# Kernel optimization log

Measured on AMD Instinct MI355X. Metric: run time of the kernel, lower is better.

## Reference

```python
import jax, jax.numpy as jnp
import numpy as np

NUM_CONVEX = 50
B, D = 16384, 2048
OOS_LABEL_ID = 150


def setup_inputs() -> dict:
    key = jax.random.key(0)
    k1, k2, k3, k4 = jax.random.split(key, 4)
    z = jax.random.normal(k1, (B, D), dtype=jnp.float32)
    label_ids = jax.random.randint(k2, (B,), 0, OOS_LABEL_ID, dtype=jnp.int64)
    data_type = jnp.zeros((B,), dtype=jnp.float32)
    # pre-sampled pair indices (rows with differing labels in the original's
    # rejection loop) and uniform mixing coefficients s ~ U(0,1)
    pair_idx = jax.random.randint(k3, (NUM_CONVEX, 2), 0, B, dtype=jnp.int64)
    s = jax.random.uniform(k4, (NUM_CONVEX,), dtype=jnp.float32)
    return {"z": z, "label_ids": label_ids, "data_type": data_type,
            "pair_idx": pair_idx, "s": s, "oos_label_id": OOS_LABEL_ID}


def reference(z, label_ids, data_type, pair_idx, s, oos_label_id):
    # convex combos: s*z[a] + (1-s)*z[b]  -> [NUM_CONVEX, D]
    za = z[pair_idx[:, 0]]
    zb = z[pair_idx[:, 1]]
    convex = s[:, None] * za + (1.0 - s[:, None]) * zb
    z_out = jnp.concatenate([z, convex], axis=0)                 # [B+50, D]
    n = s.shape[0]
    labels_out = jnp.concatenate(
        [label_ids, jnp.full((n,), oos_label_id, dtype=label_ids.dtype)])
    data_type_out = jnp.concatenate(
        [data_type, jnp.ones((n,), dtype=data_type.dtype)])
    return z_out, labels_out, data_type_out
```

## Files before the change

### kernel.cpp

```cpp
#include <hip/hip_runtime.h>


#define B_ROWS 16384
#define D_COLS 2048
#define NCONV  50
#define D4     (D_COLS / 4)
#define NZ4    (B_ROWS * D4)
#define NC4    (NCONV * D4)
#define NR     (B_ROWS + NCONV)
#define NTAIL  (2 * NR)

#define IPT          16
#define COPY_BLOCKS  (NZ4 / (256 * IPT))
#define CONV_BLOCKS  ((NC4 + 255) / 256)
#define TAIL_BLOCKS  ((NTAIL + 255) / 256)

typedef float f4 __attribute__((ext_vector_type(4)));

__global__ __launch_bounds__(256) void convex_sampler_v3(
    const float* __restrict__ z,
    const int*   __restrict__ label_ids,
    const float* __restrict__ data_type,
    const int*   __restrict__ pair_idx,
    const float* __restrict__ s,
    const int*   __restrict__ oos_label_id,
    float*       __restrict__ out)
{
    const f4* __restrict__ z4   = (const f4*)z;
    f4*       __restrict__ out4 = (f4*)out;

    const int bid = blockIdx.x;

    if (bid < COPY_BLOCKS) {
        const int base = bid * (256 * IPT) + threadIdx.x;
        f4 v[IPT];
        #pragma unroll
        for (int k = 0; k < IPT; ++k)
            v[k] = z4[base + k * 256];
        #pragma unroll
        for (int k = 0; k < IPT; ++k)
            __builtin_nontemporal_store(v[k], &out4[base + k * 256]);
        return;
    }

    if (bid < COPY_BLOCKS + CONV_BLOCKS) {
        const int j  = (bid - COPY_BLOCKS) * 256 + threadIdx.x;
        const int r  = j >> 9;
        const int c4 = j & 511;
        const int ia = pair_idx[2 * r];
        const int ib = pair_idx[2 * r + 1];
        const float sv = s[r];
        const float tv = 1.0f - sv;
        const f4 a = z4[ia * D4 + c4];
        const f4 b = z4[ib * D4 + c4];
        f4 rr;
        rr.x = sv * a.x + tv * b.x;
        rr.y = sv * a.y + tv * b.y;
        rr.z = sv * a.z + tv * b.z;
        rr.w = sv * a.w + tv * b.w;
        out4[NZ4 + j] = rr;
        return;
    }

    {
        const int t = (bid - COPY_BLOCKS - CONV_BLOCKS) * 256 + threadIdx.x;
        if (t >= NTAIL) return;
        const int base = NR * D_COLS;
        if (t < NR) {
            float v = (t < B_ROWS) ? (float)label_ids[t]
                                   : (float)(*oos_label_id);
            out[base + t] = v;
        } else {
            const int u = t - NR;
            float v = (u < B_ROWS) ? data_type[u] : 1.0f;
            out[base + NR + u] = v;
        }
    }
}

extern "C" void kernel_launch(void* const* d_in, const int* in_sizes, int n_in,
                              void* d_out, int out_size, void* d_ws, size_t ws_size,
                              hipStream_t stream) {
    const float* z          = (const float*)d_in[0];
    const int*   label_ids  = (const int*)  d_in[1];
    const float* data_type  = (const float*)d_in[2];
    const int*   pair_idx   = (const int*)  d_in[3];
    const float* s          = (const float*)d_in[4];
    const int*   oos        = (const int*)  d_in[5];
    float*       out        = (float*)d_out;

    dim3 grid(COPY_BLOCKS + CONV_BLOCKS + TAIL_BLOCKS), block(256);
    hipLaunchKernelGGL(convex_sampler_v3, grid, block, 0, stream,
                       z, label_ids, data_type, pair_idx, s, oos, out);
}
```

Baseline: 248.7 us.

## Split fused copy kernel into two half-copy launches plus a small convex/tail kernel

Replaces the single fused kernel with three launches on the same stream: two that each copy half of z into the output, and one that computes the convex combinations and writes the label and data_type tails. Per-thread work drops from 16 to 8 vectors, and the copy now uses plain stores instead of nontemporal stores. The extra launches add fixed overhead and serialize the work on one stream. Regular stores may also change cache write-back behavior for this large streaming copy.

```diff
diff --git a/kernel.cpp b/kernel.cpp
--- a/kernel.cpp
+++ b/kernel.cpp
@@ -6,18 +6,33 @@
 #define NCONV  50
 #define D4     (D_COLS / 4)
 #define NZ4    (B_ROWS * D4)
+#define HALF4  (NZ4 / 2)
 #define NC4    (NCONV * D4)
 #define NR     (B_ROWS + NCONV)
 #define NTAIL  (2 * NR)
 
-#define IPT          16
-#define COPY_BLOCKS  (NZ4 / (256 * IPT))
-#define CONV_BLOCKS  ((NC4 + 255) / 256)
-#define TAIL_BLOCKS  ((NTAIL + 255) / 256)
+#define IPT        8
+#define COPY_BLKS  (HALF4 / (256 * IPT))
+#define CONV_BLKS  ((NC4 + 255) / 256)
+#define TAIL_BLKS  ((NTAIL + 255) / 256)
+#define SMALL_BLKS (CONV_BLKS + TAIL_BLKS)
 
 typedef float f4 __attribute__((ext_vector_type(4)));
 
-__global__ __launch_bounds__(256) void convex_sampler_v3(
+__global__ __launch_bounds__(256) void copy_half(const f4* __restrict__ src,
+                                                 f4* __restrict__ dst)
+{
+    const int base = blockIdx.x * (256 * IPT) + threadIdx.x;
+    f4 v[IPT];
+    #pragma unroll
+    for (int k = 0; k < IPT; ++k)
+        v[k] = src[base + k * 256];
+    #pragma unroll
+    for (int k = 0; k < IPT; ++k)
+        dst[base + k * 256] = v[k];
+}
+
+__global__ __launch_bounds__(256) void convex_and_tails(
     const float* __restrict__ z,
     const int*   __restrict__ label_ids,
     const float* __restrict__ data_type,
@@ -28,23 +43,10 @@
 {
     const f4* __restrict__ z4   = (const f4*)z;
     f4*       __restrict__ out4 = (f4*)out;
-
     const int bid = blockIdx.x;
 
-    if (bid < COPY_BLOCKS) {
-        const int base = bid * (256 * IPT) + threadIdx.x;
-        f4 v[IPT];
-        #pragma unroll
-        for (int k = 0; k < IPT; ++k)
-            v[k] = z4[base + k * 256];
-        #pragma unroll
-        for (int k = 0; k < IPT; ++k)
-            __builtin_nontemporal_store(v[k], &out4[base + k * 256]);
-        return;
-    }
-
-    if (bid < COPY_BLOCKS + CONV_BLOCKS) {
-        const int j  = (bid - COPY_BLOCKS) * 256 + threadIdx.x;
+    if (bid < CONV_BLKS) {
+        const int j  = bid * 256 + threadIdx.x;
         const int r  = j >> 9;
         const int c4 = j & 511;
         const int ia = pair_idx[2 * r];
@@ -62,19 +64,17 @@
         return;
     }
 
-    {
-        const int t = (bid - COPY_BLOCKS - CONV_BLOCKS) * 256 + threadIdx.x;
-        if (t >= NTAIL) return;
-        const int base = NR * D_COLS;
-        if (t < NR) {
-            float v = (t < B_ROWS) ? (float)label_ids[t]
-                                   : (float)(*oos_label_id);
-            out[base + t] = v;
-        } else {
-            const int u = t - NR;
-            float v = (u < B_ROWS) ? data_type[u] : 1.0f;
-            out[base + NR + u] = v;
-        }
+    const int t = (bid - CONV_BLKS) * 256 + threadIdx.x;
+    if (t >= NTAIL) return;
+    const int base = NR * D_COLS;
+    if (t < NR) {
+        float v = (t < B_ROWS) ? (float)label_ids[t]
+                               : (float)(*oos_label_id);
+        out[base + t] = v;
+    } else {
+        const int u = t - NR;
+        float v = (u < B_ROWS) ? data_type[u] : 1.0f;
+        out[base + NR + u] = v;
     }
 }
 
@@ -89,7 +89,13 @@
     const int*   oos        = (const int*)  d_in[5];
     float*       out        = (float*)d_out;
 
-    dim3 grid(COPY_BLOCKS + CONV_BLOCKS + TAIL_BLOCKS), block(256);
-    hipLaunchKernelGGL(convex_sampler_v3, grid, block, 0, stream,
+    const f4* z4   = (const f4*)z;
+    f4*       out4 = (f4*)out;
+
+    hipLaunchKernelGGL(copy_half, dim3(COPY_BLKS), dim3(256), 0, stream,
+                       z4, out4);
+    hipLaunchKernelGGL(copy_half, dim3(COPY_BLKS), dim3(256), 0, stream,
+                       z4 + HALF4, out4 + HALF4);
+    hipLaunchKernelGGL(convex_and_tails, dim3(SMALL_BLKS), dim3(256), 0, stream,
                        z, label_ids, data_type, pair_idx, s, oos, out);
 }
```

After: 241.0 us. 3.1% less time.
